# Kernel optimization log

Measured on AMD Instinct MI355X. Metric: run time of the kernel, lower is better.

Reference implementation:

```python
import jax, jax.numpy as jnp
import numpy as np

N = 50000
E = 400000
F_IN = 5
H = 8
C1, C2, C3 = 64, 32, 16
NEG_SLOPE = 0.2


def setup_inputs() -> dict:
    key = jax.random.key(0)
    ks = jax.random.split(key, 16)
    s = 0.1  # small init scale
    return {
        "x": jax.random.normal(ks[0], (N, F_IN), jnp.float32),
        "edge_index": jax.random.randint(ks[1], (2, E), 0, N, jnp.int64),
        "edge_weight": jax.random.uniform(ks[2], (E,), jnp.float32),
        "W1": jax.random.normal(ks[3], (F_IN, H * C1), jnp.float32) * s,
        "a_src1": jax.random.normal(ks[4], (H, C1), jnp.float32) * s,
        "a_dst1": jax.random.normal(ks[5], (H, C1), jnp.float32) * s,
        "b1": jnp.zeros((H * C1,), jnp.float32),
        "W2": jax.random.normal(ks[6], (H * C1, H * C2), jnp.float32) * s,
        "a_src2": jax.random.normal(ks[7], (H, C2), jnp.float32) * s,
        "a_dst2": jax.random.normal(ks[8], (H, C2), jnp.float32) * s,
        "b2": jnp.zeros((H * C2,), jnp.float32),
        "Wg": jax.random.normal(ks[9], (H * C2, C3), jnp.float32) * s,
        "bg": jnp.zeros((C3,), jnp.float32),
        "Wfc": jax.random.normal(ks[10], (C3, 1), jnp.float32) * s,
        "bfc": jnp.zeros((1,), jnp.float32),
    }


def _gat_layer(x, W, a_src, a_dst, b, src, dst, n, heads, ch):
    # PyG GATConv (concat=True), eval mode (dropout off), self-loops already in src/dst.
    h = (x @ W).reshape(n, heads, ch)                      # (N, H, C)
    e_s = jnp.sum(h * a_src, axis=-1)                      # (N, H)
    e_d = jnp.sum(h * a_dst, axis=-1)                      # (N, H)
    e = jax.nn.leaky_relu(e_s[src] + e_d[dst], NEG_SLOPE)  # (Etot, H)
    m = jax.ops.segment_max(e, dst, num_segments=n)
    m = jnp.where(jnp.isfinite(m), m, 0.0)                 # guard empty segments
    ex = jnp.exp(e - m[dst])
    den = jax.ops.segment_sum(ex, dst, num_segments=n)
    alpha = ex / (den[dst] + 1e-16)                        # softmax over in-edges
    out = jax.ops.segment_sum(h[src] * alpha[..., None], dst, num_segments=n)
    return out.reshape(n, heads * ch) + b


def _gcn_layer(x, W, b, src, dst, w_full, n):
    # PyG GCNConv with gcn_norm: D^{-1/2} A_hat D^{-1/2}, self-loop weight 1.
    deg = jax.ops.segment_sum(w_full, dst, num_segments=n)
    dinv = jnp.where(deg > 0, jax.lax.rsqrt(deg), 0.0)
    norm = dinv[src] * w_full * dinv[dst]                  # (Etot,)
    h = x @ W                                              # (N, C3)
    out = jax.ops.segment_sum(h[src] * norm[:, None], dst, num_segments=n)
    return out + b


def reference(x, edge_index, edge_weight, W1, a_src1, a_dst1, b1,
              W2, a_src2, a_dst2, b2, Wg, bg, Wfc, bfc):
    n = x.shape[0]
    loops = jnp.arange(n, dtype=edge_index.dtype)
    src = jnp.concatenate([edge_index[0], loops])
    dst = jnp.concatenate([edge_index[1], loops])
    w_full = jnp.concatenate([edge_weight, jnp.ones((n,), edge_weight.dtype)])

    h = _gat_layer(x, W1, a_src1, a_dst1, b1, src, dst, n, H, C1)
    h = jax.nn.elu(h)
    h = _gat_layer(h, W2, a_src2, a_dst2, b2, src, dst, n, H, C2)
    h = jax.nn.elu(h)
    h = _gcn_layer(h, Wg, bg, src, dst, w_full, n)
    h = jax.nn.elu(h)
    out = jax.nn.sigmoid(h @ Wfc + bfc)                    # (N, 1)
    return out
```

## Files before the change

### kernel.cpp

```cpp
#include <hip/hip_runtime.h>
#include <hip/hip_bf16.h>
#include <float.h>
#include <math.h>

#define N_NODES 50000
#define N_EDGES 400000
#define ETOT    (N_EDGES + N_NODES)
#define F_IN    5
#define HEADS   8
#define C1      64
#define C2      32
#define C3      16
#define HC1     (HEADS * C1)
#define HC2     (HEADS * C2)
#define H2S     (HC2 + 16)
#define NEG_SLOPE 0.2f
#define NCHUNK  ((N_NODES + 255) / 256)
#define NH8     (N_NODES * HEADS)
#define MPAD    (((N_NODES + 63) / 64) * 64)
#define GCOLS   (HC2 + 16)
#define PACKBLK ((GCOLS * HC1) / 256)
#define SCATBLK ((ETOT + 255) / 256)
#define ES1BLK  ((NH8 + 255) / 256)
#define INIT_DEG  ((N_EDGES + 255) / 256)
#define INIT_W2X  (INIT_DEG + PACKBLK)
#define INIT_TOT  (INIT_W2X + ES1BLK)

#define WFIX_SCALE 68719476736.0f
#define WFIX_MASK  ((1ULL << 46) - 1)

typedef short bf16x8 __attribute__((ext_vector_type(8)));
typedef float f32x4  __attribute__((ext_vector_type(4)));
typedef unsigned short ushort_t;
typedef unsigned short ushort8_t __attribute__((ext_vector_type(8)));

__device__ __forceinline__ float eluf(float x) {
    return x > 0.f ? x : (expf(x) - 1.f);
}
__device__ __forceinline__ float bf2f(unsigned short u) {
    union { unsigned int i; float f; } v; v.i = ((unsigned int)u) << 16; return v.f;
}
__device__ __forceinline__ unsigned short f2bf(float f) {
    __hip_bfloat16 b = __float2bfloat16(f);
    return *(unsigned short*)&b;
}
__device__ __forceinline__ float softnum(float es, float ed) {
    float v = es + ed;
    v = v > 0.f ? v : NEG_SLOPE * v;
    return expf(v);
}

__global__ void k_init(const int* __restrict__ ei, const float* __restrict__ ew,
                       unsigned long long* __restrict__ pack,
                       ushort_t* __restrict__ rank,
                       const float* __restrict__ x, float* __restrict__ xp8,
                       const float* __restrict__ W2,
                       const float* __restrict__ a_src2, const float* __restrict__ a_dst2,
                       ushort_t* __restrict__ W2X,
                       const float* __restrict__ W1,
                       const float* __restrict__ a_src1, const float* __restrict__ a_dst1,
                       float* __restrict__ es, float* __restrict__ ed) {
    __shared__ float asl[HEADS * F_IN], adl[HEADS * F_IN];
    int b = blockIdx.x;
    int t = threadIdx.x;
    if (b < INIT_DEG) {
        int i = b * 256 + t;
        if (i >= N_EDGES) return;
        int d   = ei[N_EDGES + i];
        float w = ew[i];
        unsigned long long enc =
            (1ULL << 46) | (unsigned long long)(w * WFIX_SCALE + 0.5f);
        unsigned long long old = atomicAdd(&pack[d], enc);
        rank[i] = (ushort_t)(old >> 46);
    } else if (b < INIT_W2X) {
        int idx = (b - INIT_DEG) * 256 + t;
        int c = idx >> 9;
        int k = idx & 511;
        float v;
        if (c < HC2) {
            v = W2[(size_t)k * HC2 + c];
        } else {
            int h = (c - HC2) & 7;
            const float* av = (c < HC2 + 8) ? a_src2 : a_dst2;
            v = 0.f;
#pragma unroll 8
            for (int j = 0; j < C2; j++)
                v += W2[(size_t)k * HC2 + h * C2 + j] * av[h * C2 + j];
        }
        W2X[idx] = f2bf(v);
    } else {
        if (t < HEADS * F_IN) {
            int h = t / F_IN, f = t % F_IN;
            float s = 0.f, dv = 0.f;
            for (int c = 0; c < C1; c++) {
                float wv = W1[f * HC1 + h * C1 + c];
                s  += wv * a_src1[h * C1 + c];
                dv += wv * a_dst1[h * C1 + c];
            }
            asl[t] = s;
            adl[t] = dv;
        }
        __syncthreads();
        int g = (b - INIT_W2X) * 256 + t;
        if (g < NH8) {
            int n = g >> 3, h = g & 7;
            float vs = 0.f, vd = 0.f;
#pragma unroll
            for (int f = 0; f < F_IN; f++) {
                float xv = x[n * F_IN + f];
                vs += xv * asl[h * F_IN + f];
                vd += xv * adl[h * F_IN + f];
            }
            es[g] = vs;
            ed[g] = vd;
            xp8[g] = (h < F_IN) ? x[n * F_IN + h] : 0.f;
        }
    }
}

__global__ void k_scan_a(const unsigned long long* __restrict__ pack,
                         int* __restrict__ part) {
    __shared__ int lds[256];
    int t = threadIdx.x;
    int i = blockIdx.x * 256 + t;
    lds[t] = (i < N_NODES) ? (int)(pack[i] >> 46) + 1 : 0;
    __syncthreads();
    for (int off = 128; off >= 1; off >>= 1) {
        if (t < off) lds[t] += lds[t + off];
        __syncthreads();
    }
    if (t == 0) part[blockIdx.x] = lds[0];
}

__global__ void k_scan_b(int* part) {
    __shared__ int lds[256];
    int t = threadIdx.x;
    int v = (t < NCHUNK) ? part[t] : 0;
    lds[t] = v;
    __syncthreads();
    for (int off = 1; off < 256; off <<= 1) {
        int x = (t >= off) ? lds[t - off] : 0;
        __syncthreads();
        lds[t] += x;
        __syncthreads();
    }
    if (t < NCHUNK) part[t] = lds[t] - v;
}

__global__ void k_scan_c(const unsigned long long* __restrict__ pack,
                         const int* __restrict__ part,
                         int* __restrict__ offs, float* __restrict__ dinv) {
    __shared__ int lds[256];
    int t = threadIdx.x;
    int i = blockIdx.x * 256 + t;
    unsigned long long p = (i < N_NODES) ? pack[i] : 0ULL;
    int v = (i < N_NODES) ? (int)(p >> 46) + 1 : 0;
    lds[t] = v;
    __syncthreads();
    for (int off = 1; off < 256; off <<= 1) {
        int x = (t >= off) ? lds[t - off] : 0;
        __syncthreads();
        lds[t] += x;
        __syncthreads();
    }
    int excl = part[blockIdx.x] + lds[t] - v;
    if (i < N_NODES) {
        offs[i] = excl;
        float wsum = (float)(p & WFIX_MASK) * (1.0f / WFIX_SCALE) + 1.0f;
        dinv[i] = rsqrtf(wsum);
    }
    if (i == N_NODES - 1) offs[N_NODES] = excl + v;
}

__global__ void k_scatter(const int* __restrict__ ei, const int* __restrict__ offs,
                          const ushort_t* __restrict__ rank, int2* __restrict__ csr,
                          const float* __restrict__ ew, const float* __restrict__ dinv) {
    int i = blockIdx.x * 256 + threadIdx.x;
    if (i >= ETOT) return;
    int s, d, pos;
    float w;
    if (i < N_EDGES) {
        s = ei[i]; d = ei[N_EDGES + i]; w = ew[i];
        pos = offs[d] + (int)rank[i];
    } else {
        s = d = i - N_EDGES; w = 1.f;
        pos = offs[d + 1] - 1;
    }
    float nrm = dinv[s] * w * dinv[d];
    csr[pos] = make_int2(s, __float_as_int(nrm));
}

__global__ __launch_bounds__(256) void k_aggexp(const float* __restrict__ xp8,
                                                const float* __restrict__ es1,
                                                const float* __restrict__ ed1,
                                                const int* __restrict__ offs,
                                                const int2* __restrict__ csr,
                                                const float* __restrict__ W1,
                                                const float* __restrict__ b1,
                                                ushort_t* __restrict__ x2bf) {
    __shared__ float ax[256 * F_IN];
    int t = threadIdx.x;
    int g = blockIdx.x * 256 + t;
    if (g < NH8) {
        int d = g >> 3, h = g & 7;
        float edv = ed1[g];
        int k0 = offs[d], k1 = offs[d + 1];
        float a0 = 0.f, a1 = 0.f, a2 = 0.f, a3 = 0.f, a4 = 0.f, exsum = 0.f;
        int k = k0;
        for (; k + 3 < k1; k += 4) {
            int2 c0 = csr[k], c1 = csr[k + 1], c2 = csr[k + 2], c3 = csr[k + 3];
            float r0 = es1[c0.x * HEADS + h];
            float r1 = es1[c1.x * HEADS + h];
            float r2 = es1[c2.x * HEADS + h];
            float r3 = es1[c3.x * HEADS + h];
            float4 A0 = *(const float4*)(xp8 + (size_t)c0.x * 8);
            float  B0 = xp8[(size_t)c0.x * 8 + 4];
            float4 A1 = *(const float4*)(xp8 + (size_t)c1.x * 8);
            float  B1 = xp8[(size_t)c1.x * 8 + 4];
            float4 A2 = *(const float4*)(xp8 + (size_t)c2.x * 8);
            float  B2 = xp8[(size_t)c2.x * 8 + 4];
            float4 A3 = *(const float4*)(xp8 + (size_t)c3.x * 8);
            float  B3 = xp8[(size_t)c3.x * 8 + 4];
            float x0 = softnum(r0, edv);
            float x1 = softnum(r1, edv);
            float x2 = softnum(r2, edv);
            float x3 = softnum(r3, edv);
            a0 += x0 * A0.x + x1 * A1.x + x2 * A2.x + x3 * A3.x;
            a1 += x0 * A0.y + x1 * A1.y + x2 * A2.y + x3 * A3.y;
            a2 += x0 * A0.z + x1 * A1.z + x2 * A2.z + x3 * A3.z;
            a3 += x0 * A0.w + x1 * A1.w + x2 * A2.w + x3 * A3.w;
            a4 += x0 * B0   + x1 * B1   + x2 * B2   + x3 * B3;
            exsum += (x0 + x1) + (x2 + x3);
        }
        for (; k < k1; k++) {
            int2 c0 = csr[k];
            float x0 = softnum(es1[c0.x * HEADS + h], edv);
            float4 A0 = *(const float4*)(xp8 + (size_t)c0.x * 8);
            float  B0 = xp8[(size_t)c0.x * 8 + 4];
            a0 += x0 * A0.x;
            a1 += x0 * A0.y;
            a2 += x0 * A0.z;
            a3 += x0 * A0.w;
            a4 += x0 * B0;
            exsum += x0;
        }
        float inv = 1.f / (exsum + 1e-16f);
        float* ap = ax + t * F_IN;
        ap[0] = a0 * inv;
        ap[1] = a1 * inv;
        ap[2] = a2 * inv;
        ap[3] = a3 * inv;
        ap[4] = a4 * inv;
    }
    __syncthreads();
    int wave = t >> 6, j = t & 63;
    int n0 = blockIdx.x * 32;
    int h = j >> 3;
    const float* w1p = W1 + j * 8;
#pragma unroll 1
    for (int it = 0; it < 8; ++it) {
        int nl = wave * 8 + it;
        int n = n0 + nl;
        if (n >= N_NODES) break;
        const float* ap = ax + (nl * 8 + h) * F_IN;
        float av[F_IN];
#pragma unroll
        for (int f = 0; f < F_IN; f++) av[f] = ap[f];
        float4 s0 = *(const float4*)(b1 + j * 8);
        float4 s1 = *(const float4*)(b1 + j * 8 + 4);
#pragma unroll
        for (int f = 0; f < F_IN; f++) {
            float4 w0  = *(const float4*)(w1p + f * HC1);
            float4 w1v = *(const float4*)(w1p + f * HC1 + 4);
            s0.x += av[f] * w0.x;  s0.y += av[f] * w0.y;
            s0.z += av[f] * w0.z;  s0.w += av[f] * w0.w;
            s1.x += av[f] * w1v.x; s1.y += av[f] * w1v.y;
            s1.z += av[f] * w1v.z; s1.w += av[f] * w1v.w;
        }
        ushort8_t o;
        o[0] = f2bf(eluf(s0.x)); o[1] = f2bf(eluf(s0.y));
        o[2] = f2bf(eluf(s0.z)); o[3] = f2bf(eluf(s0.w));
        o[4] = f2bf(eluf(s1.x)); o[5] = f2bf(eluf(s1.y));
        o[6] = f2bf(eluf(s1.z)); o[7] = f2bf(eluf(s1.w));
        *(ushort8_t*)(x2bf + (size_t)n * HC1 + j * 8) = o;
    }
}

__global__ __launch_bounds__(256, 3) void k_gemm_mfma(const short* __restrict__ A,
                                                      const short* __restrict__ W2X,
                                                      ushort_t* __restrict__ h2x,
                                                      float* __restrict__ ed2) {
    __shared__ short Bs[GCOLS * 32];
    int t    = threadIdx.x;
    int wave = t >> 6;
    int lane = t & 63;
    int lo   = lane & 15;
    int quad = lane >> 4;
    int m0   = blockIdx.x * 64 + wave * 16;
    const short* ap = A + (size_t)(m0 + lo) * HC1 + quad * 8;

    f32x4 acc[17];
#pragma unroll
    for (int f = 0; f < 17; f++) acc[f] = (f32x4){0.f, 0.f, 0.f, 0.f};

    for (int idx = t; idx < GCOLS * 4; idx += 256) {
        int c = idx >> 2, q = idx & 3;
        int s = (q + c + (c >> 2)) & 3;
        *(bf16x8*)(Bs + c * 32 + s * 8) = *(const bf16x8*)(W2X + (size_t)c * HC1 + q * 8);
    }
    __syncthreads();

#pragma unroll 1
    for (int k0 = 0; k0 < HC1; k0 += 32) {
        int nk = k0 + 32;
        bf16x8 pre[5];
        if (nk < HC1) {
#pragma unroll
            for (int j = 0; j < 5; j++) {
                int idx = t + j * 256;
                if (idx < GCOLS * 4) {
                    int c = idx >> 2, q = idx & 3;
                    pre[j] = *(const bf16x8*)(W2X + (size_t)c * HC1 + nk + q * 8);
                }
            }
        }
        bf16x8 aF = *(const bf16x8*)(ap + k0);
#pragma unroll
        for (int f = 0; f < 17; f++) {
            int c = f * 16 + lo;
            int s = (quad + c + (c >> 2)) & 3;
            bf16x8 bF = *(const bf16x8*)(Bs + c * 32 + s * 8);
            acc[f] = __builtin_amdgcn_mfma_f32_16x16x32_bf16(aF, bF, acc[f], 0, 0, 0);
        }
        __syncthreads();
        if (nk < HC1) {
#pragma unroll
            for (int j = 0; j < 5; j++) {
                int idx = t + j * 256;
                if (idx < GCOLS * 4) {
                    int c = idx >> 2, q = idx & 3;
                    int s = (q + c + (c >> 2)) & 3;
                    *(bf16x8*)(Bs + c * 32 + s * 8) = pre[j];
                }
            }
            __syncthreads();
        }
    }

    int rowb = m0 + quad * 4;
#pragma unroll
    for (int f = 0; f < 16; f++) {
#pragma unroll
        for (int r = 0; r < 4; r++) {
            int row = rowb + r;
            if (row < N_NODES)
                h2x[(size_t)row * H2S + f * 16 + lo] = f2bf(acc[f][r]);
        }
    }
#pragma unroll
    for (int r = 0; r < 4; r++) {
        int row = rowb + r;
        if (row < N_NODES) {
            if (lo < 8) *(float*)(h2x + (size_t)row * H2S + HC2 + 2 * lo) = acc[16][r];
            else        ed2[row * HEADS + (lo - 8)] = acc[16][r];
        }
    }
}

__global__ __launch_bounds__(128) void k_gat_agg2(const ushort_t* __restrict__ h2x,
                                                  const float* __restrict__ ed2,
                                                  const int* __restrict__ offs,
                                                  const int2* __restrict__ csr,
                                                  const float* __restrict__ b2,
                                                  ushort_t* __restrict__ x3bf) {
    int wave = threadIdx.x >> 6;
    int lane = threadIdx.x & 63;
    int d = blockIdx.x * 2 + wave;
    if (d >= N_NODES) return;
    int c4 = lane * 4;
    int h  = lane >> 3;
    float edv = ed2[d * HEADS + h];
    int k0 = offs[d], k1 = offs[d + 1];
    float acc0 = 0.f, acc1 = 0.f, acc2 = 0.f, acc3 = 0.f, exsum = 0.f;
    int k = k0;
    for (; k + 3 < k1; k += 4) {
        int2 e0 = csr[k], e1 = csr[k + 1], e2 = csr[k + 2], e3 = csr[k + 3];
        const ushort_t* p0 = h2x + (size_t)e0.x * H2S;
        const ushort_t* p1 = h2x + (size_t)e1.x * H2S;
        const ushort_t* p2 = h2x + (size_t)e2.x * H2S;
        const ushort_t* p3 = h2x + (size_t)e3.x * H2S;
        float r0 = *(const float*)(p0 + HC2 + 2 * h);
        float r1 = *(const float*)(p1 + HC2 + 2 * h);
        float r2 = *(const float*)(p2 + HC2 + 2 * h);
        float r3 = *(const float*)(p3 + HC2 + 2 * h);
        ushort4 v0 = *(const ushort4*)(p0 + c4);
        ushort4 v1 = *(const ushort4*)(p1 + c4);
        ushort4 v2 = *(const ushort4*)(p2 + c4);
        ushort4 v3 = *(const ushort4*)(p3 + c4);
        float x0 = softnum(r0, edv);
        float x1 = softnum(r1, edv);
        float x2 = softnum(r2, edv);
        float x3 = softnum(r3, edv);
        acc0 += x0 * bf2f(v0.x) + x1 * bf2f(v1.x) + x2 * bf2f(v2.x) + x3 * bf2f(v3.x);
        acc1 += x0 * bf2f(v0.y) + x1 * bf2f(v1.y) + x2 * bf2f(v2.y) + x3 * bf2f(v3.y);
        acc2 += x0 * bf2f(v0.z) + x1 * bf2f(v1.z) + x2 * bf2f(v2.z) + x3 * bf2f(v3.z);
        acc3 += x0 * bf2f(v0.w) + x1 * bf2f(v1.w) + x2 * bf2f(v2.w) + x3 * bf2f(v3.w);
        exsum += (x0 + x1) + (x2 + x3);
    }
    for (; k < k1; k++) {
        int2 e0 = csr[k];
        const ushort_t* p0 = h2x + (size_t)e0.x * H2S;
        float x0 = softnum(*(const float*)(p0 + HC2 + 2 * h), edv);
        ushort4 v0 = *(const ushort4*)(p0 + c4);
        acc0 += x0 * bf2f(v0.x);
        acc1 += x0 * bf2f(v0.y);
        acc2 += x0 * bf2f(v0.z);
        acc3 += x0 * bf2f(v0.w);
        exsum += x0;
    }
    float inv = 1.f / (exsum + 1e-16f);
    float4 bias = *(const float4*)(b2 + c4);
    ushort4 o;
    o.x = f2bf(eluf(acc0 * inv + bias.x));
    o.y = f2bf(eluf(acc1 * inv + bias.y));
    o.z = f2bf(eluf(acc2 * inv + bias.z));
    o.w = f2bf(eluf(acc3 * inv + bias.w));
    *(ushort4*)(x3bf + (size_t)d * HC2 + c4) = o;
}

__global__ __launch_bounds__(256) void k_hg(const ushort_t* __restrict__ x3bf,
                                            const float* __restrict__ Wg,
                                            float* __restrict__ hg) {
    __shared__ float xs[16 * 260];
    int n0 = blockIdx.x * 16;
    int t  = threadIdx.x;
    for (int q = t; q < 16 * HC2 / 4; q += 256) {
        int r  = q >> 6;
        int cc = (q & 63) * 4;
        int n  = n0 + r;
        ushort4 v = make_ushort4(0, 0, 0, 0);
        if (n < N_NODES) v = *(const ushort4*)(x3bf + (size_t)n * HC2 + cc);
        xs[r * 260 + cc + 0] = bf2f(v.x);
        xs[r * 260 + cc + 1] = bf2f(v.y);
        xs[r * 260 + cc + 2] = bf2f(v.z);
        xs[r * 260 + cc + 3] = bf2f(v.w);
    }
    __syncthreads();
    int r = t >> 4, c = t & 15;
    const float* xr = xs + r * 260;
    float acc = 0.f;
#pragma unroll 8
    for (int k = 0; k < HC2; k += 4) {
        float4 v = *(const float4*)(xr + k);
        acc += v.x * Wg[(k + 0) * C3 + c];
        acc += v.y * Wg[(k + 1) * C3 + c];
        acc += v.z * Wg[(k + 2) * C3 + c];
        acc += v.w * Wg[(k + 3) * C3 + c];
    }
    int n = n0 + r;
    if (n < N_NODES) hg[(size_t)n * C3 + c] = acc;
}

__global__ __launch_bounds__(256) void k_gcn_out(const float* __restrict__ hg,
                                                 const int* __restrict__ offs,
                                                 const int2* __restrict__ csr,
                                                 const float* __restrict__ bg,
                                                 const float* __restrict__ Wfc,
                                                 const float* __restrict__ bfc,
                                                 float* __restrict__ out) {
    int t = threadIdx.x;
    int r = t >> 4, c = t & 15;
    int d = blockIdx.x * 16 + r;
    float val = 0.f;
    if (d < N_NODES) {
        int k0 = offs[d], k1 = offs[d + 1];
        float acc = 0.f;
        int k = k0;
        for (; k + 3 < k1; k += 4) {
            int2 e0 = csr[k], e1 = csr[k + 1], e2 = csr[k + 2], e3 = csr[k + 3];
            float g0 = hg[(size_t)e0.x * C3 + c];
            float g1 = hg[(size_t)e1.x * C3 + c];
            float g2 = hg[(size_t)e2.x * C3 + c];
            float g3 = hg[(size_t)e3.x * C3 + c];
            acc += g0 * __int_as_float(e0.y) + g1 * __int_as_float(e1.y)
                 + g2 * __int_as_float(e2.y) + g3 * __int_as_float(e3.y);
        }
        for (; k < k1; k++) {
            int2 e0 = csr[k];
            acc += hg[(size_t)e0.x * C3 + c] * __int_as_float(e0.y);
        }
        val = eluf(acc + bg[c]);
    }
    float z = val * Wfc[c];
#pragma unroll
    for (int off = 8; off >= 1; off >>= 1) z += __shfl_xor(z, off, 16);
    if (c == 0 && d < N_NODES) out[d] = 1.f / (1.f + expf(-(z + bfc[0])));
}

extern "C" void kernel_launch(void* const* d_in, const int* in_sizes, int n_in,
                              void* d_out, int out_size, void* d_ws, size_t ws_size,
                              hipStream_t stream) {
    const float* x       = (const float*)d_in[0];
    const int*   ei      = (const int*)  d_in[1];
    const float* ew      = (const float*)d_in[2];
    const float* W1      = (const float*)d_in[3];
    const float* a_src1  = (const float*)d_in[4];
    const float* a_dst1  = (const float*)d_in[5];
    const float* b1      = (const float*)d_in[6];
    const float* W2      = (const float*)d_in[7];
    const float* a_src2  = (const float*)d_in[8];
    const float* a_dst2  = (const float*)d_in[9];
    const float* b2      = (const float*)d_in[10];
    const float* Wg      = (const float*)d_in[11];
    const float* bg      = (const float*)d_in[12];
    const float* Wfc     = (const float*)d_in[13];
    const float* bfc     = (const float*)d_in[14];
    float* out = (float*)d_out;

    char* w = (char*)d_ws;
    size_t off = 0;
    auto alloc = [&](size_t bytes) -> void* {
        void* p = w + off;
        off = (off + bytes + 255) & ~(size_t)255;
        return p;
    };
    ushort_t* x2bf = (ushort_t*)alloc((size_t)MPAD * HC1 * 2);
    ushort_t* W2X  = (ushort_t*)alloc((size_t)GCOLS * HC1 * 2);
    ushort_t* h2x  = (ushort_t*)alloc((size_t)N_NODES * H2S * 2);
    ushort_t* x3bf = (ushort_t*)alloc((size_t)N_NODES * HC2 * 2);
    float* hg     = (float*)alloc((size_t)N_NODES * C3 * 4);
    float* es1    = (float*)alloc((size_t)NH8 * 4);
    float* ed1    = (float*)alloc((size_t)NH8 * 4);
    float* ed2    = (float*)alloc((size_t)NH8 * 4);
    unsigned long long* pack = (unsigned long long*)alloc((size_t)N_NODES * 8);
    char*  zero_end = w + off;
    ushort_t* rank = (ushort_t*)alloc((size_t)N_EDGES * 2);
    int*   offs   = (int*)  alloc((size_t)(N_NODES + 1) * 4);
    int*   part   = (int*)  alloc(256 * 4);
    int2*  csr    = (int2*) alloc((size_t)ETOT * 8);
    float* dinv   = (float*)alloc((size_t)N_NODES * 4);
    float* xp8    = (float*)alloc((size_t)N_NODES * 8 * 4);

    hipMemsetAsync(pack, 0, (size_t)(zero_end - (char*)pack), stream);
    k_init<<<dim3(INIT_TOT), dim3(256), 0, stream>>>(
        ei, ew, pack, rank, x, xp8, W2, a_src2, a_dst2, W2X,
        W1, a_src1, a_dst1, es1, ed1);
    k_scan_a<<<dim3(NCHUNK), dim3(256), 0, stream>>>(pack, part);
    k_scan_b<<<dim3(1), dim3(256), 0, stream>>>(part);
    k_scan_c<<<dim3(NCHUNK), dim3(256), 0, stream>>>(pack, part, offs, dinv);
    k_scatter<<<dim3(SCATBLK), dim3(256), 0, stream>>>(ei, offs, rank, csr, ew, dinv);

    k_aggexp<<<dim3(ES1BLK), dim3(256), 0, stream>>>(
        xp8, es1, ed1, offs, csr, W1, b1, x2bf);

    k_gemm_mfma<<<dim3(MPAD / 64), dim3(256), 0, stream>>>(
        (const short*)x2bf, (const short*)W2X, h2x, ed2);
    k_gat_agg2<<<dim3((N_NODES + 1) / 2), dim3(128), 0, stream>>>(
        h2x, ed2, offs, csr, b2, x3bf);

    k_hg<<<dim3((N_NODES + 15) / 16), dim3(256), 0, stream>>>(x3bf, Wg, hg);
    k_gcn_out<<<dim3((N_NODES + 15) / 16), dim3(256), 0, stream>>>(
        hg, offs, csr, bg, Wfc, bfc, out);
}
```

Baseline: 277.5 us.

## Move layer-1 expansion into GEMM kernel via shared memory, split aggregation out

The layer-1 aggregation now writes a compact 5-feature-per-head buffer. A new kernel expands it through W1, bias and ELU directly into a swizzled shared-memory bf16 tile and feeds it to the MFMA GEMM. This avoids writing and re-reading the full 512-column bf16 intermediate in global memory. Each block now covers 32 rows, with the 17 output fragments split across wave pairs, which doubles the grid and recomputes the cheap expansion per block. The tile costs 32 KB of LDS, which may lower occupancy.

After: 303.9 us. 1.1x slower.

```diff
diff --git a/kernel.cpp b/kernel.cpp
--- a/kernel.cpp
+++ b/kernel.cpp
@@ -17,7 +17,6 @@
 #define NEG_SLOPE 0.2f
 #define NCHUNK  ((N_NODES + 255) / 256)
 #define NH8     (N_NODES * HEADS)
-#define MPAD    (((N_NODES + 63) / 64) * 64)
 #define GCOLS   (HC2 + 16)
 #define PACKBLK ((GCOLS * HC1) / 256)
 #define SCATBLK ((ETOT + 255) / 256)
@@ -190,118 +189,122 @@
     csr[pos] = make_int2(s, __float_as_int(nrm));
 }
 
-__global__ __launch_bounds__(256) void k_aggexp(const float* __restrict__ xp8,
-                                                const float* __restrict__ es1,
-                                                const float* __restrict__ ed1,
-                                                const int* __restrict__ offs,
-                                                const int2* __restrict__ csr,
-                                                const float* __restrict__ W1,
-                                                const float* __restrict__ b1,
-                                                ushort_t* __restrict__ x2bf) {
-    __shared__ float ax[256 * F_IN];
+__global__ void k_agg(const float* __restrict__ xp8,
+                      const float* __restrict__ es1, const float* __restrict__ ed1,
+                      const int* __restrict__ offs, const int2* __restrict__ csr,
+                      float* __restrict__ aggx) {
+    int g = blockIdx.x * blockDim.x + threadIdx.x;
+    if (g >= NH8) return;
+    int d = g >> 3, h = g & 7;
+    float edv = ed1[g];
+    int k0 = offs[d], k1 = offs[d + 1];
+    float a0 = 0.f, a1 = 0.f, a2 = 0.f, a3 = 0.f, a4 = 0.f, exsum = 0.f;
+    int k = k0;
+    for (; k + 3 < k1; k += 4) {
+        int2 c0 = csr[k], c1 = csr[k + 1], c2 = csr[k + 2], c3 = csr[k + 3];
+        float r0 = es1[c0.x * HEADS + h];
+        float r1 = es1[c1.x * HEADS + h];
+        float r2 = es1[c2.x * HEADS + h];
+        float r3 = es1[c3.x * HEADS + h];
+        float4 A0 = *(const float4*)(xp8 + (size_t)c0.x * 8);
+        float  B0 = xp8[(size_t)c0.x * 8 + 4];
+        float4 A1 = *(const float4*)(xp8 + (size_t)c1.x * 8);
+        float  B1 = xp8[(size_t)c1.x * 8 + 4];
+        float4 A2 = *(const float4*)(xp8 + (size_t)c2.x * 8);
+        float  B2 = xp8[(size_t)c2.x * 8 + 4];
+        float4 A3 = *(const float4*)(xp8 + (size_t)c3.x * 8);
+        float  B3 = xp8[(size_t)c3.x * 8 + 4];
+        float x0 = softnum(r0, edv);
+        float x1 = softnum(r1, edv);
+        float x2 = softnum(r2, edv);
+        float x3 = softnum(r3, edv);
+        a0 += x0 * A0.x + x1 * A1.x + x2 * A2.x + x3 * A3.x;
+        a1 += x0 * A0.y + x1 * A1.y + x2 * A2.y + x3 * A3.y;
+        a2 += x0 * A0.z + x1 * A1.z + x2 * A2.z + x3 * A3.z;
+        a3 += x0 * A0.w + x1 * A1.w + x2 * A2.w + x3 * A3.w;
+        a4 += x0 * B0   + x1 * B1   + x2 * B2   + x3 * B3;
+        exsum += (x0 + x1) + (x2 + x3);
+    }
+    for (; k < k1; k++) {
+        int2 c0 = csr[k];
+        float x0 = softnum(es1[c0.x * HEADS + h], edv);
+        float4 A0 = *(const float4*)(xp8 + (size_t)c0.x * 8);
+        float  B0 = xp8[(size_t)c0.x * 8 + 4];
+        a0 += x0 * A0.x;
+        a1 += x0 * A0.y;
+        a2 += x0 * A0.z;
+        a3 += x0 * A0.w;
+        a4 += x0 * B0;
+        exsum += x0;
+    }
+    float inv = 1.f / (exsum + 1e-16f);
+    aggx[0 * NH8 + g] = a0 * inv;
+    aggx[1 * NH8 + g] = a1 * inv;
+    aggx[2 * NH8 + g] = a2 * inv;
+    aggx[3 * NH8 + g] = a3 * inv;
+    aggx[4 * NH8 + g] = a4 * inv;
+}
+
+__global__ __launch_bounds__(256, 3) void k_expgemm(const float* __restrict__ aggx,
+                                                    const float* __restrict__ W1,
+                                                    const float* __restrict__ b1,
+                                                    const short* __restrict__ W2X,
+                                                    ushort_t* __restrict__ h2x,
+                                                    float* __restrict__ ed2) {
+    __shared__ short xs2[32 * HC1];
+    __shared__ short Bs[GCOLS * 32];
     int t = threadIdx.x;
-    int g = blockIdx.x * 256 + t;
-    if (g < NH8) {
-        int d = g >> 3, h = g & 7;
-        float edv = ed1[g];
-        int k0 = offs[d], k1 = offs[d + 1];
-        float a0 = 0.f, a1 = 0.f, a2 = 0.f, a3 = 0.f, a4 = 0.f, exsum = 0.f;
-        int k = k0;
-        for (; k + 3 < k1; k += 4) {
-            int2 c0 = csr[k], c1 = csr[k + 1], c2 = csr[k + 2], c3 = csr[k + 3];
-            float r0 = es1[c0.x * HEADS + h];
-            float r1 = es1[c1.x * HEADS + h];
-            float r2 = es1[c2.x * HEADS + h];
-            float r3 = es1[c3.x * HEADS + h];
-            float4 A0 = *(const float4*)(xp8 + (size_t)c0.x * 8);
-            float  B0 = xp8[(size_t)c0.x * 8 + 4];
-            float4 A1 = *(const float4*)(xp8 + (size_t)c1.x * 8);
-            float  B1 = xp8[(size_t)c1.x * 8 + 4];
-            float4 A2 = *(const float4*)(xp8 + (size_t)c2.x * 8);
-            float  B2 = xp8[(size_t)c2.x * 8 + 4];
-            float4 A3 = *(const float4*)(xp8 + (size_t)c3.x * 8);
-            float  B3 = xp8[(size_t)c3.x * 8 + 4];
-            float x0 = softnum(r0, edv);
-            float x1 = softnum(r1, edv);
-            float x2 = softnum(r2, edv);
-            float x3 = softnum(r3, edv);
-            a0 += x0 * A0.x + x1 * A1.x + x2 * A2.x + x3 * A3.x;
-            a1 += x0 * A0.y + x1 * A1.y + x2 * A2.y + x3 * A3.y;
-            a2 += x0 * A0.z + x1 * A1.z + x2 * A2.z + x3 * A3.z;
-            a3 += x0 * A0.w + x1 * A1.w + x2 * A2.w + x3 * A3.w;
-            a4 += x0 * B0   + x1 * B1   + x2 * B2   + x3 * B3;
-            exsum += (x0 + x1) + (x2 + x3);
-        }
-        for (; k < k1; k++) {
-            int2 c0 = csr[k];
-            float x0 = softnum(es1[c0.x * HEADS + h], edv);
-            float4 A0 = *(const float4*)(xp8 + (size_t)c0.x * 8);
-            float  B0 = xp8[(size_t)c0.x * 8 + 4];
-            a0 += x0 * A0.x;
-            a1 += x0 * A0.y;
-            a2 += x0 * A0.z;
-            a3 += x0 * A0.w;
-            a4 += x0 * B0;
-            exsum += x0;
-        }
-        float inv = 1.f / (exsum + 1e-16f);
-        float* ap = ax + t * F_IN;
-        ap[0] = a0 * inv;
-        ap[1] = a1 * inv;
-        ap[2] = a2 * inv;
-        ap[3] = a3 * inv;
-        ap[4] = a4 * inv;
+
+    {
+        int wave = t >> 6, j = t & 63;
+        int h = j >> 3;
+        const float* w1p = W1 + j * 8;
+#pragma unroll 1
+        for (int it = 0; it < 8; ++it) {
+            int nl = wave * 8 + it;
+            int n = blockIdx.x * 32 + nl;
+            ushort8_t o;
+            if (n < N_NODES) {
+                int g = n * HEADS + h;
+                float av[F_IN];
+#pragma unroll
+                for (int f = 0; f < F_IN; f++) av[f] = aggx[f * NH8 + g];
+                float4 s0 = *(const float4*)(b1 + j * 8);
+                float4 s1 = *(const float4*)(b1 + j * 8 + 4);
+#pragma unroll
+                for (int f = 0; f < F_IN; f++) {
+                    float4 w0  = *(const float4*)(w1p + f * HC1);
+                    float4 w1v = *(const float4*)(w1p + f * HC1 + 4);
+                    s0.x += av[f] * w0.x;  s0.y += av[f] * w0.y;
+                    s0.z += av[f] * w0.z;  s0.w += av[f] * w0.w;
+                    s1.x += av[f] * w1v.x; s1.y += av[f] * w1v.y;
+                    s1.z += av[f] * w1v.z; s1.w += av[f] * w1v.w;
+                }
+                o[0] = f2bf(eluf(s0.x)); o[1] = f2bf(eluf(s0.y));
+                o[2] = f2bf(eluf(s0.z)); o[3] = f2bf(eluf(s0.w));
+                o[4] = f2bf(eluf(s1.x)); o[5] = f2bf(eluf(s1.y));
+                o[6] = f2bf(eluf(s1.z)); o[7] = f2bf(eluf(s1.w));
+            } else {
+                for (int q = 0; q < 8; q++) o[q] = 0;
+            }
+            int scol = (j * 8) ^ ((nl & 7) << 3);
+            *(ushort8_t*)(xs2 + nl * HC1 + scol) = *(ushort8_t*)&o;
+        }
     }
     __syncthreads();
-    int wave = t >> 6, j = t & 63;
-    int n0 = blockIdx.x * 32;
-    int h = j >> 3;
-    const float* w1p = W1 + j * 8;
-#pragma unroll 1
-    for (int it = 0; it < 8; ++it) {
-        int nl = wave * 8 + it;
-        int n = n0 + nl;
-        if (n >= N_NODES) break;
-        const float* ap = ax + (nl * 8 + h) * F_IN;
-        float av[F_IN];
-#pragma unroll
-        for (int f = 0; f < F_IN; f++) av[f] = ap[f];
-        float4 s0 = *(const float4*)(b1 + j * 8);
-        float4 s1 = *(const float4*)(b1 + j * 8 + 4);
-#pragma unroll
-        for (int f = 0; f < F_IN; f++) {
-            float4 w0  = *(const float4*)(w1p + f * HC1);
-            float4 w1v = *(const float4*)(w1p + f * HC1 + 4);
-            s0.x += av[f] * w0.x;  s0.y += av[f] * w0.y;
-            s0.z += av[f] * w0.z;  s0.w += av[f] * w0.w;
-            s1.x += av[f] * w1v.x; s1.y += av[f] * w1v.y;
-            s1.z += av[f] * w1v.z; s1.w += av[f] * w1v.w;
-        }
-        ushort8_t o;
-        o[0] = f2bf(eluf(s0.x)); o[1] = f2bf(eluf(s0.y));
-        o[2] = f2bf(eluf(s0.z)); o[3] = f2bf(eluf(s0.w));
-        o[4] = f2bf(eluf(s1.x)); o[5] = f2bf(eluf(s1.y));
-        o[6] = f2bf(eluf(s1.z)); o[7] = f2bf(eluf(s1.w));
-        *(ushort8_t*)(x2bf + (size_t)n * HC1 + j * 8) = o;
-    }
-}
-
-__global__ __launch_bounds__(256, 3) void k_gemm_mfma(const short* __restrict__ A,
-                                                      const short* __restrict__ W2X,
-                                                      ushort_t* __restrict__ h2x,
-                                                      float* __restrict__ ed2) {
-    __shared__ short Bs[GCOLS * 32];
-    int t    = threadIdx.x;
+
     int wave = t >> 6;
     int lane = t & 63;
     int lo   = lane & 15;
     int quad = lane >> 4;
-    int m0   = blockIdx.x * 64 + wave * 16;
-    const short* ap = A + (size_t)(m0 + lo) * HC1 + quad * 8;
-
-    f32x4 acc[17];
-#pragma unroll
-    for (int f = 0; f < 17; f++) acc[f] = (f32x4){0.f, 0.f, 0.f, 0.f};
+    int rg   = (wave & 1) * 16;
+    int half = wave >> 1;
+    int f0   = half ? 9 : 0;
+    int nf   = half ? 8 : 9;
+
+    f32x4 acc[9];
+#pragma unroll
+    for (int f = 0; f < 9; f++) acc[f] = (f32x4){0.f, 0.f, 0.f, 0.f};
 
     for (int idx = t; idx < GCOLS * 4; idx += 256) {
         int c = idx >> 2, q = idx & 3;
@@ -324,13 +327,17 @@
                 }
             }
         }
-        bf16x8 aF = *(const bf16x8*)(ap + k0);
-#pragma unroll
-        for (int f = 0; f < 17; f++) {
-            int c = f * 16 + lo;
-            int s = (quad + c + (c >> 2)) & 3;
-            bf16x8 bF = *(const bf16x8*)(Bs + c * 32 + s * 8);
-            acc[f] = __builtin_amdgcn_mfma_f32_16x16x32_bf16(aF, bF, acc[f], 0, 0, 0);
+        int arow = rg + lo;
+        int aelem = (k0 + quad * 8) ^ ((arow & 7) << 3);
+        bf16x8 aF = *(const bf16x8*)(xs2 + arow * HC1 + aelem);
+#pragma unroll
+        for (int f = 0; f < 9; f++) {
+            if (f < nf) {
+                int c = (f0 + f) * 16 + lo;
+                int s = (quad + c + (c >> 2)) & 3;
+                bf16x8 bF = *(const bf16x8*)(Bs + c * 32 + s * 8);
+                acc[f] = __builtin_amdgcn_mfma_f32_16x16x32_bf16(aF, bF, acc[f], 0, 0, 0);
+            }
         }
         __syncthreads();
         if (nk < HC1) {
@@ -347,22 +354,28 @@
         }
     }
 
-    int rowb = m0 + quad * 4;
-#pragma unroll
-    for (int f = 0; f < 16; f++) {
-#pragma unroll
-        for (int r = 0; r < 4; r++) {
-            int row = rowb + r;
-            if (row < N_NODES)
-                h2x[(size_t)row * H2S + f * 16 + lo] = f2bf(acc[f][r]);
-        }
-    }
-#pragma unroll
-    for (int r = 0; r < 4; r++) {
-        int row = rowb + r;
-        if (row < N_NODES) {
-            if (lo < 8) *(float*)(h2x + (size_t)row * H2S + HC2 + 2 * lo) = acc[16][r];
-            else        ed2[row * HEADS + (lo - 8)] = acc[16][r];
+    int rowb = blockIdx.x * 32 + rg + quad * 4;
+#pragma unroll
+    for (int f = 0; f < 9; f++) {
+        if (f < nf) {
+            int af = f0 + f;
+            if (af < 16) {
+#pragma unroll
+                for (int r = 0; r < 4; r++) {
+                    int row = rowb + r;
+                    if (row < N_NODES)
+                        h2x[(size_t)row * H2S + af * 16 + lo] = f2bf(acc[f][r]);
+                }
+            } else {
+#pragma unroll
+                for (int r = 0; r < 4; r++) {
+                    int row = rowb + r;
+                    if (row < N_NODES) {
+                        if (lo < 8) *(float*)(h2x + (size_t)row * H2S + HC2 + 2 * lo) = acc[f][r];
+                        else        ed2[row * HEADS + (lo - 8)] = acc[f][r];
+                    }
+                }
+            }
         }
     }
 }
@@ -524,11 +537,11 @@
         off = (off + bytes + 255) & ~(size_t)255;
         return p;
     };
-    ushort_t* x2bf = (ushort_t*)alloc((size_t)MPAD * HC1 * 2);
     ushort_t* W2X  = (ushort_t*)alloc((size_t)GCOLS * HC1 * 2);
     ushort_t* h2x  = (ushort_t*)alloc((size_t)N_NODES * H2S * 2);
     ushort_t* x3bf = (ushort_t*)alloc((size_t)N_NODES * HC2 * 2);
     float* hg     = (float*)alloc((size_t)N_NODES * C3 * 4);
+    float* aggx   = (float*)alloc((size_t)F_IN * NH8 * 4);
     float* es1    = (float*)alloc((size_t)NH8 * 4);
     float* ed1    = (float*)alloc((size_t)NH8 * 4);
     float* ed2    = (float*)alloc((size_t)NH8 * 4);
@@ -550,11 +563,10 @@
     k_scan_c<<<dim3(NCHUNK), dim3(256), 0, stream>>>(pack, part, offs, dinv);
     k_scatter<<<dim3(SCATBLK), dim3(256), 0, stream>>>(ei, offs, rank, csr, ew, dinv);
 
-    k_aggexp<<<dim3(ES1BLK), dim3(256), 0, stream>>>(
-        xp8, es1, ed1, offs, csr, W1, b1, x2bf);
-
-    k_gemm_mfma<<<dim3(MPAD / 64), dim3(256), 0, stream>>>(
-        (const short*)x2bf, (const short*)W2X, h2x, ed2);
+    k_agg<<<dim3(ES1BLK), dim3(256), 0, stream>>>(xp8, es1, ed1, offs, csr, aggx);
+    k_expgemm<<<dim3(ES1BLK), dim3(256), 0, stream>>>(
+        aggx, W1, b1, (const short*)W2X, h2x, ed2);
+
     k_gat_agg2<<<dim3((N_NODES + 1) / 2), dim3(128), 0, stream>>>(
         h2x, ed2, offs, csr, b2, x3bf);
 
```
